# Kernel tuning notes

Measured on AMD Instinct MI355X. Metric: run time of the kernel, lower is better.

The kernel has to match this reference:

```python
import jax, jax.numpy as jnp
import numpy as np
import math

NUM_HEADS = 16
ROPE_BASE = 10000.0


def _rope_cos_sin(seq_len, head_dim, dtype):
    # Qwen2-style rotary embeddings. The torch source builds cos/sin of width
    # head_dim by concatenating freqs with itself, so the first and second
    # halves are identical; the half-width table below is the equivalent math.
    half = head_dim // 2
    inv_freq = 1.0 / (ROPE_BASE ** (jnp.arange(0, head_dim, 2, dtype=jnp.float32) / head_dim))
    t = jnp.arange(seq_len, dtype=jnp.float32)
    freqs = jnp.einsum('i,j->ij', t, inv_freq)  # [S, half]
    cos = jnp.cos(freqs).astype(dtype)[None, None]  # [1,1,S,half]
    sin = jnp.sin(freqs).astype(dtype)[None, None]
    return cos, sin


def _apply_rope(x, cos, sin):
    # x: [B, H, S, D]; split-half rotation (Qwen2 rotate-half convention)
    half = x.shape[-1] // 2
    x1, x2 = x[..., :half], x[..., half:]
    return jnp.concatenate([x1 * cos - x2 * sin, x2 * cos + x1 * sin], axis=-1)


def setup_inputs() -> dict:
    key = jax.random.key(0)
    ks = jax.random.split(key, 5)
    B, S, H = 2, 2048, 2048
    scale = 1.0 / math.sqrt(H)
    return {
        'hidden_states': jax.random.normal(ks[0], (B, S, H), dtype=jnp.float32),
        'Wq': jax.random.normal(ks[1], (H, H), dtype=jnp.float32) * scale,
        'Wk': jax.random.normal(ks[2], (H, H), dtype=jnp.float32) * scale,
        'Wv': jax.random.normal(ks[3], (H, H), dtype=jnp.float32) * scale,
        'Wo': jax.random.normal(ks[4], (H, H), dtype=jnp.float32) * scale,
    }


def reference(hidden_states, Wq, Wk, Wv, Wo):
    B, S, H = hidden_states.shape
    nh = NUM_HEADS
    hd = H // nh

    def proj(W):
        # nn.Linear: x @ W.T ; then [B,S,H] -> [B,nh,S,hd]
        y = jnp.einsum('bsh,oh->bso', hidden_states, W)
        return y.reshape(B, S, nh, hd).transpose(0, 2, 1, 3)

    q, k, v = proj(Wq), proj(Wk), proj(Wv)

    cos, sin = _rope_cos_sin(S, hd, hidden_states.dtype)
    q = _apply_rope(q, cos, sin)
    k = _apply_rope(k, cos, sin)

    scores = jnp.einsum('bhqd,bhkd->bhqk', q, k) / math.sqrt(hd)
    causal = jnp.triu(jnp.full((S, S), -jnp.inf, dtype=scores.dtype), k=1)
    scores = scores + causal[None, None]
    probs = jax.nn.softmax(scores, axis=-1)

    ctx = jnp.einsum('bhqk,bhkd->bhqd', probs, v)  # [B,nh,S,hd]
    ctx = ctx.transpose(0, 2, 1, 3).reshape(B, S, H)
    out = jnp.einsum('bsh,oh->bso', ctx, Wo)
    return out
```

## Files before the change

### kernel.cpp

```cpp
#include <hip/hip_runtime.h>

#define S_LEN 2048
#define HID   2048
#define NHEAD 16
#define HD    128
#define BSZ   2
#define BS_TOT (BSZ * S_LEN)
#define QKS   4096

typedef __bf16 bf16x8 __attribute__((ext_vector_type(8)));
typedef unsigned short u16x8 __attribute__((ext_vector_type(8)));
typedef unsigned short u16x4 __attribute__((ext_vector_type(4)));
typedef float f32x4 __attribute__((ext_vector_type(4)));

static __device__ __forceinline__ bf16x8 as_bf(u16x8 v) { return __builtin_bit_cast(bf16x8, v); }

static __device__ __forceinline__ unsigned short f2bf(float f) {
  __bf16 h = (__bf16)f;
  return __builtin_bit_cast(unsigned short, h);
}
static __device__ __forceinline__ float bf2f(unsigned short b) {
  unsigned int u = ((unsigned int)b) << 16;
  return __builtin_bit_cast(float, u);
}

static __device__ __forceinline__ void gload_lds16(const unsigned short* g, unsigned short* l) {
  __builtin_amdgcn_global_load_lds((const __attribute__((address_space(1))) unsigned int*)g,
                                   (__attribute__((address_space(3))) unsigned int*)l, 16, 0, 0);
}

__global__ __launch_bounds__(256) void cvt_all(const float* __restrict__ hs,
                                               const float* __restrict__ Wq,
                                               const float* __restrict__ Wk,
                                               const float* __restrict__ Wv,
                                               const float* __restrict__ Wo,
                                               unsigned short* __restrict__ hsb,
                                               unsigned short* __restrict__ wall,
                                               float* __restrict__ ct, float* __restrict__ st) {
  int b = (int)blockIdx.x, tid = (int)threadIdx.x;
  if (b < 8192) {
    int i = b * 256 + tid;
    float4 v = ((const float4*)hs)[i];
    ushort4 o; o.x = f2bf(v.x); o.y = f2bf(v.y); o.z = f2bf(v.z); o.w = f2bf(v.w);
    ((ushort4*)hsb)[i] = o;
  } else if (b < 24576) {
    int t = b - 8192;
    int wsel = t >> 12;
    const float* in = (wsel == 0) ? Wq : (wsel == 1) ? Wk : (wsel == 2) ? Wv : Wo;
    int i = (t & 4095) * 256 + tid;
    float4 v = ((const float4*)in)[i];
    ushort4 o; o.x = f2bf(v.x); o.y = f2bf(v.y); o.z = f2bf(v.z); o.w = f2bf(v.w);
    ((ushort4*)(wall + (size_t)wsel * HID * HID))[i] = o;
  } else {
    int id = (b - 24576) * 256 + tid;
    int tt = id >> 6, d = id & 63;
    float inv = powf(10000.0f, -(float)d * (1.0f / 64.0f));
    float f = (float)tt * inv;
    float sv, cv;
    sincosf(f, &sv, &cv);
    ct[id] = cv; st[id] = sv;
  }
}

__global__ __launch_bounds__(256) void rope_apply_k(unsigned short* __restrict__ qk,
                                                    const float* __restrict__ ct,
                                                    const float* __restrict__ st) {
  int id = blockIdx.x * 256 + threadIdx.x;
  int d4 = (id & 15) * 4;
  int h = (id >> 4) & (NHEAD - 1);
  int m = id >> 8;
  int s = m & (S_LEN - 1);
  float4 c  = *(const float4*)(ct + s * 64 + d4);
  float4 sn = *(const float4*)(st + s * 64 + d4);
  size_t base = (size_t)m * QKS + 2048 + h * HD + d4;
  u16x4 k1 = *(u16x4*)(qk + base), k2 = *(u16x4*)(qk + base + 64);
  u16x4 p1, p2;
  float cc[4] = {c.x, c.y, c.z, c.w}, ss[4] = {sn.x, sn.y, sn.z, sn.w};
#pragma unroll
  for (int j = 0; j < 4; ++j) {
    float ak = bf2f(k1[j]), bk = bf2f(k2[j]);
    p1[j] = f2bf(ak * cc[j] - bk * ss[j]);
    p2[j] = f2bf(bk * cc[j] + ak * ss[j]);
  }
  *(u16x4*)(qk + base) = p1;
  *(u16x4*)(qk + base + 64) = p2;
}

template <typename OutT>
__global__ __launch_bounds__(512, 1) void gemm256(const unsigned short* __restrict__ A,
                                                  const unsigned short* __restrict__ Bw,
                                                  OutT* __restrict__ C, int M, int N, int K) {
  __shared__ __align__(16) unsigned short As[2][256 * 64];
  __shared__ __align__(16) unsigned short Bs[2][256 * 64];
  int x = (int)blockIdx.x;
  int chunk = (int)gridDim.x >> 3;
  int x2 = (x & 7) * chunk + (x >> 3);
  const int nbn = N >> 8;
  int bm = x2 / nbn, bn = x2 % nbn;
  int tid = (int)threadIdx.x;
  int l = tid & 63, lr = l & 15, lg = l >> 4;
  int w = tid >> 6;
  int wm = w >> 2, wn = w & 3;

  int srow = 32 * w + (l >> 3);
  int sslot = (l & 7) ^ ((l >> 3) & 7);
  const unsigned short* gA = A + (size_t)(bm * 256 + srow) * K + sslot * 8;
  const unsigned short* gB = Bw + (size_t)(bn * 256 + srow) * K + sslot * 8;

  int rs7 = lr & 7;

  f32x4 zero = {0.f, 0.f, 0.f, 0.f};
  f32x4 acc[8][4];
#pragma unroll
  for (int mi = 0; mi < 8; ++mi)
#pragma unroll
    for (int ni = 0; ni < 4; ++ni) acc[mi][ni] = zero;

  int nk = K >> 6;

#define STAGE256(buf, kt)                                                       \
  do {                                                                          \
    size_t ko_ = (size_t)(kt) * 64;                                             \
    _Pragma("unroll") for (int i_ = 0; i_ < 4; ++i_) {                          \
      gload_lds16(gA + (size_t)(8 * i_) * K + ko_, &As[buf][(32 * w + 8 * i_) * 64]); \
      gload_lds16(gB + (size_t)(8 * i_) * K + ko_, &Bs[buf][(32 * w + 8 * i_) * 64]); \
    }                                                                           \
  } while (0)

  STAGE256(0, 0);
  __syncthreads();

  for (int kt = 0; kt < nk; ++kt) {
    if (kt + 1 < nk) STAGE256((kt + 1) & 1, kt + 1);
    const unsigned short* Ab = &As[kt & 1][0];
    const unsigned short* Bb = &Bs[kt & 1][0];

    u16x8 bfr[4][2];
#pragma unroll
    for (int ni = 0; ni < 4; ++ni)
#pragma unroll
      for (int ks = 0; ks < 2; ++ks)
        bfr[ni][ks] = *(const u16x8*)&Bb[(wn * 64 + ni * 16 + lr) * 64 + (((ks * 4 + lg) ^ rs7) * 8)];

#pragma unroll
    for (int mq = 0; mq < 4; ++mq) {
      u16x8 af[2][2];
#pragma unroll
      for (int m2 = 0; m2 < 2; ++m2)
#pragma unroll
        for (int ks = 0; ks < 2; ++ks)
          af[m2][ks] = *(const u16x8*)&Ab[(wm * 128 + (2 * mq + m2) * 16 + lr) * 64 + (((ks * 4 + lg) ^ rs7) * 8)];
      __builtin_amdgcn_s_setprio(1);
#pragma unroll
      for (int m2 = 0; m2 < 2; ++m2)
#pragma unroll
        for (int ni = 0; ni < 4; ++ni)
#pragma unroll
          for (int ks = 0; ks < 2; ++ks)
            acc[2 * mq + m2][ni] = __builtin_amdgcn_mfma_f32_16x16x32_bf16(
                as_bf(af[m2][ks]), as_bf(bfr[ni][ks]), acc[2 * mq + m2][ni], 0, 0, 0);
      __builtin_amdgcn_s_setprio(0);
      __builtin_amdgcn_s_barrier();
    }
    __syncthreads();
  }
#undef STAGE256

#pragma unroll
  for (int mi = 0; mi < 8; ++mi) {
#pragma unroll
    for (int ni = 0; ni < 4; ++ni) {
      int col = bn * 256 + wn * 64 + ni * 16 + lr;
#pragma unroll
      for (int j = 0; j < 4; ++j) {
        int rowm = bm * 256 + wm * 128 + mi * 16 + 4 * lg + j;
        float v = acc[mi][ni][j];
        if constexpr (sizeof(OutT) == 2) C[(size_t)rowm * N + col] = f2bf(v);
        else                             C[(size_t)rowm * N + col] = v;
      }
    }
  }
  (void)M;
}

template <typename OutT>
__global__ __launch_bounds__(256) void gemm128(const unsigned short* __restrict__ A,
                                               const unsigned short* __restrict__ Bw,
                                               OutT* __restrict__ C, int M, int N, int K) {
  __shared__ __align__(16) unsigned short As[4][128 * 32];
  __shared__ __align__(16) unsigned short Bs[4][128 * 32];
  int x = (int)blockIdx.x;
  int chunk = (int)gridDim.x >> 3;
  int x2 = (x & 7) * chunk + (x >> 3);
  const int nbn = N >> 7;
  int bm = x2 / nbn, bn = x2 % nbn;
  int tid = (int)threadIdx.x;
  int l = tid & 63, lr = l & 15, lg = l >> 4;
  int w = tid >> 6, wm = w >> 1, wn = w & 1;

  int w32 = 32 * w;
  int srow = w32 + (l >> 2);
  int ssw = ((l >> 2) ^ (l >> 4)) & 3;
  const unsigned short* gA = A + (size_t)(bm * 128 + srow) * K + (((l & 3) ^ ssw) << 3);
  const unsigned short* gB = Bw + (size_t)(bn * 128 + srow) * K + (((l & 3) ^ ssw) << 3);

  int rsw = (lr ^ (lr >> 2)) & 3;
  int aoff[4], boff[4];
#pragma unroll
  for (int i = 0; i < 4; ++i) {
    aoff[i] = (wm * 64 + i * 16 + lr) * 32 + ((lg ^ rsw) << 3);
    boff[i] = (wn * 64 + i * 16 + lr) * 32 + ((lg ^ rsw) << 3);
  }

  f32x4 zero = {0.f, 0.f, 0.f, 0.f};
  f32x4 acc[4][4];
#pragma unroll
  for (int mi = 0; mi < 4; ++mi)
#pragma unroll
    for (int ni = 0; ni < 4; ++ni) acc[mi][ni] = zero;

  int nk = K >> 5;

#define STAGE(buf, kt)                                                        \
  do {                                                                        \
    const unsigned short* pa_ = gA + (size_t)(kt) * 32;                       \
    const unsigned short* pb_ = gB + (size_t)(kt) * 32;                       \
    gload_lds16(pa_, &As[buf][w32 * 32]);                                     \
    gload_lds16(pa_ + (size_t)16 * K, &As[buf][(w32 + 16) * 32]);             \
    gload_lds16(pb_, &Bs[buf][w32 * 32]);                                     \
    gload_lds16(pb_ + (size_t)16 * K, &Bs[buf][(w32 + 16) * 32]);             \
  } while (0)

#define COMPUTE(buf)                                                          \
  do {                                                                        \
    u16x8 af[4], bfr[4];                                                      \
    _Pragma("unroll") for (int i = 0; i < 4; ++i) {                           \
      af[i] = *(const u16x8*)&As[buf][aoff[i]];                               \
      bfr[i] = *(const u16x8*)&Bs[buf][boff[i]];                              \
    }                                                                         \
    _Pragma("unroll") for (int mi = 0; mi < 4; ++mi)                          \
        _Pragma("unroll") for (int ni = 0; ni < 4; ++ni)                      \
            acc[mi][ni] = __builtin_amdgcn_mfma_f32_16x16x32_bf16(            \
                as_bf(af[mi]), as_bf(bfr[ni]), acc[mi][ni], 0, 0, 0);         \
  } while (0)

  STAGE(0, 0);
  STAGE(1, 1);
  STAGE(2, 2);
  asm volatile("s_waitcnt vmcnt(8)" ::: "memory");
  __builtin_amdgcn_s_barrier();
#pragma unroll 4
  for (int kt = 0; kt < nk; ++kt) {
    COMPUTE(kt & 3);
    asm volatile("s_waitcnt vmcnt(4) lgkmcnt(0)" ::: "memory");
    __builtin_amdgcn_s_barrier();
    STAGE((kt + 3) & 3, (kt + 3) & (nk - 1));
  }
#undef STAGE
#undef COMPUTE

#pragma unroll
  for (int mi = 0; mi < 4; ++mi) {
#pragma unroll
    for (int ni = 0; ni < 4; ++ni) {
      int col = bn * 128 + wn * 64 + ni * 16 + lr;
#pragma unroll
      for (int j = 0; j < 4; ++j) {
        int rowm = bm * 128 + wm * 64 + mi * 16 + 4 * lg + j;
        float v = acc[mi][ni][j];
        if constexpr (sizeof(OutT) == 2) C[(size_t)rowm * N + col] = f2bf(v);
        else                             C[(size_t)rowm * N + col] = v;
      }
    }
  }
  (void)M;
}

__global__ __launch_bounds__(256, 2) void attn_fwd(const unsigned short* __restrict__ qk,
                                                   const unsigned short* __restrict__ vt,
                                                   unsigned short* __restrict__ ctx,
                                                   const float* __restrict__ ct,
                                                   const float* __restrict__ st) {
  __shared__ __align__(16) unsigned short Ks[2][64 * 128];
  __shared__ __align__(16) unsigned short Vs[2][128 * 64];
  __shared__ __align__(16) unsigned short Ps[4 * 32 * 64];

  int x = (int)blockIdx.x;
  int bh, qt;
  if (x < 256) { bh = x & 31;         qt = 15 - (x >> 5); }
  else         { bh = (x - 256) & 31; qt = (x - 256) >> 5; }
  int b = bh >> 4, h = bh & 15;
  int q0 = qt * 128;
  int nt = 2 * qt + 2;

  int tid = (int)threadIdx.x;
  int w = tid >> 6, l = tid & 63, lr = l & 15, lg = l >> 4;
  const float CEXP = 0.12751744f;
  const float MB   = -23.0831391f;
  const int bS = b * S_LEN, h128 = h * HD;
  const int qw = q0 + w * 32;
  const unsigned short* qg = qk;
  const unsigned short* kg = qk + 2048;

  u16x8 qfr[2][4];
#pragma unroll
  for (int qf = 0; qf < 2; ++qf) {
    const unsigned short* qb = qg + (size_t)(bS + qw + qf * 16 + lr) * QKS + h128;
#pragma unroll
    for (int kk = 0; kk < 4; ++kk) qfr[qf][kk] = *(const u16x8*)(qb + kk * 32 + lg * 8);
    int spos = qw + qf * 16 + lr;
#pragma unroll
    for (int kk = 0; kk < 2; ++kk) {
      int d0 = kk * 32 + lg * 8;
      float4 c0 = *(const float4*)(ct + spos * 64 + d0);
      float4 c1 = *(const float4*)(ct + spos * 64 + d0 + 4);
      float4 s0 = *(const float4*)(st + spos * 64 + d0);
      float4 s1 = *(const float4*)(st + spos * 64 + d0 + 4);
      float cc[8] = {c0.x, c0.y, c0.z, c0.w, c1.x, c1.y, c1.z, c1.w};
      float sv[8] = {s0.x, s0.y, s0.z, s0.w, s1.x, s1.y, s1.z, s1.w};
      u16x8 lo = qfr[qf][kk], hi = qfr[qf][kk + 2];
#pragma unroll
      for (int j = 0; j < 8; ++j) {
        float a = bf2f(lo[j]), b2 = bf2f(hi[j]);
        lo[j] = f2bf(a * cc[j] - b2 * sv[j]);
        hi[j] = f2bf(b2 * cc[j] + a * sv[j]);
      }
      qfr[qf][kk] = lo; qfr[qf][kk + 2] = hi;
    }
  }

  const unsigned short* kbg[4];
  const unsigned short* vbg[4];
#pragma unroll
  for (int i = 0; i < 4; ++i) {
    int rr = 16 * w + 4 * i + (l >> 4);
    int colK = ((l & 15) ^ (rr & 15)) * 8;
    kbg[i] = kg + (size_t)(bS + rr) * QKS + h128 + colK;
    int vd = 32 * w + 8 * i + (l >> 3);
    int colV = ((l & 7) ^ (vd & 7)) * 8;
    vbg[i] = vt + (size_t)(h128 + vd) * BS_TOT + bS + colV;
  }

#define ASTAGE(buf, t)                                                        \
  do {                                                                        \
    size_t koff_ = (size_t)(t) * 64 * QKS;                                    \
    int voff_ = (t) * 64;                                                     \
    _Pragma("unroll") for (int i_ = 0; i_ < 4; ++i_) {                        \
      gload_lds16(kbg[i_] + koff_, &Ks[buf][(16 * w + 4 * i_) * 128]);        \
      gload_lds16(vbg[i_] + voff_, &Vs[buf][(32 * w + 8 * i_) * 64]);         \
    }                                                                         \
  } while (0)

  f32x4 zero = {0.f, 0.f, 0.f, 0.f};
  f32x4 oacc[2][8];
#pragma unroll
  for (int qf = 0; qf < 2; ++qf)
#pragma unroll
    for (int nj = 0; nj < 8; ++nj) oacc[qf][nj] = zero;
  float lsum[2] = {0.f, 0.f};

  int cur = 0;
  ASTAGE(0, 0);
  __syncthreads();

  for (int t = 0; t < nt; ++t) {
    int k0 = t * 64;
    if (t + 1 < nt) ASTAGE(cur ^ 1, t + 1);

    if (k0 <= qw + 31) {
      const unsigned short* KsB = &Ks[cur][0];
      const unsigned short* VsB = &Vs[cur][0];

      f32x4 sac[2][4];
#pragma unroll
      for (int qf = 0; qf < 2; ++qf)
#pragma unroll
        for (int ni = 0; ni < 4; ++ni) sac[qf][ni] = zero;
      __builtin_amdgcn_s_setprio(1);
#pragma unroll
      for (int kk = 0; kk < 4; ++kk) {
#pragma unroll
        for (int ni = 0; ni < 4; ++ni) {
          u16x8 kf = *(const u16x8*)&KsB[(ni * 16 + lr) * 128 + (((kk * 4 + lg) ^ lr) * 8)];
          sac[0][ni] = __builtin_amdgcn_mfma_f32_16x16x32_bf16(as_bf(kf), as_bf(qfr[0][kk]), sac[0][ni], 0, 0, 0);
          sac[1][ni] = __builtin_amdgcn_mfma_f32_16x16x32_bf16(as_bf(kf), as_bf(qfr[1][kk]), sac[1][ni], 0, 0, 0);
        }
      }
      __builtin_amdgcn_s_setprio(0);

      u16x8 vfr[2][8];
#pragma unroll
      for (int kk2 = 0; kk2 < 2; ++kk2)
#pragma unroll
        for (int nj = 0; nj < 8; ++nj)
          vfr[kk2][nj] = *(const u16x8*)&VsB[(nj * 16 + lr) * 64 + (((kk2 * 4 + lg) ^ (lr & 7)) * 8)];

      bool needmask = (k0 + 63 > qw);
      unsigned short* pw = &Ps[w * 2048];

#pragma unroll
      for (int qf = 0; qf < 2; ++qf) {
        float s[4][4];
#pragma unroll
        for (int ni = 0; ni < 4; ++ni)
#pragma unroll
          for (int j = 0; j < 4; ++j) s[ni][j] = sac[qf][ni][j];
        if (needmask) {
          int qgl = qw + qf * 16 + lr;
#pragma unroll
          for (int ni = 0; ni < 4; ++ni)
#pragma unroll
            for (int j = 0; j < 4; ++j)
              if (k0 + ni * 16 + 4 * lg + j > qgl) s[ni][j] = -1e30f;
        }
        float rs = 0.f;
#pragma unroll
        for (int ni = 0; ni < 4; ++ni)
#pragma unroll
          for (int j = 0; j < 4; ++j) {
            float p = exp2f(fmaf(s[ni][j], CEXP, MB));
            s[ni][j] = p; rs += p;
          }
        lsum[qf] += rs;
#pragma unroll
        for (int ni = 0; ni < 4; ++ni) {
          u16x4 pv = {f2bf(s[ni][0]), f2bf(s[ni][1]), f2bf(s[ni][2]), f2bf(s[ni][3])};
          *(u16x4*)&pw[(qf * 16 + lr) * 64 + (((2 * ni + (lg >> 1)) ^ (lr & 7)) * 8) + (lg & 1) * 4] = pv;
        }
        __builtin_amdgcn_s_setprio(1);
#pragma unroll
        for (int kk2 = 0; kk2 < 2; ++kk2) {
          u16x8 pa = *(const u16x8*)&pw[(qf * 16 + lr) * 64 + (((kk2 * 4 + lg) ^ (lr & 7)) * 8)];
#pragma unroll
          for (int nj = 0; nj < 8; ++nj)
            oacc[qf][nj] = __builtin_amdgcn_mfma_f32_16x16x32_bf16(as_bf(pa), as_bf(vfr[kk2][nj]), oacc[qf][nj], 0, 0, 0);
        }
        __builtin_amdgcn_s_setprio(0);
      }
    }

    __syncthreads();
    cur ^= 1;
  }
#undef ASTAGE

#pragma unroll
  for (int qf = 0; qf < 2; ++qf) {
    float ls = lsum[qf];
    ls += __shfl_xor(ls, 16);
    ls += __shfl_xor(ls, 32);
    float rl = 1.0f / ls;
    float r0 = __shfl(rl, 4 * lg + 0, 16);
    float r1 = __shfl(rl, 4 * lg + 1, 16);
    float r2 = __shfl(rl, 4 * lg + 2, 16);
    float r3 = __shfl(rl, 4 * lg + 3, 16);
    size_t obase = (size_t)(bS + qw + qf * 16 + 4 * lg) * HID + h128;
#pragma unroll
    for (int nj = 0; nj < 8; ++nj) {
      ctx[obase + 0 * HID + nj * 16 + lr] = f2bf(oacc[qf][nj][0] * r0);
      ctx[obase + 1 * HID + nj * 16 + lr] = f2bf(oacc[qf][nj][1] * r1);
      ctx[obase + 2 * HID + nj * 16 + lr] = f2bf(oacc[qf][nj][2] * r2);
      ctx[obase + 3 * HID + nj * 16 + lr] = f2bf(oacc[qf][nj][3] * r3);
    }
  }
}

extern "C" void kernel_launch(void* const* d_in, const int* in_sizes, int n_in,
                              void* d_out, int out_size, void* d_ws, size_t ws_size,
                              hipStream_t stream) {
  const float* hs = (const float*)d_in[0];
  const float* Wq = (const float*)d_in[1];
  const float* Wk = (const float*)d_in[2];
  const float* Wv = (const float*)d_in[3];
  const float* Wo = (const float*)d_in[4];

  char* ws = (char*)d_ws;
  unsigned short* hsb  = (unsigned short*)(ws);
  unsigned short* wall = (unsigned short*)(ws + 16777216);
  unsigned short* qkb  = (unsigned short*)(ws + 50331648);
  unsigned short* vtb  = (unsigned short*)(ws + 83886080);
  float* ctab = (float*)(ws + 100663296);
  float* stab = (float*)(ws + 101187584);
  unsigned short* ctxb = hsb;

  cvt_all<<<25088, 256, 0, stream>>>(hs, Wq, Wk, Wv, Wo, hsb, wall, ctab, stab);

  gemm256<unsigned short><<<256, 512, 0, stream>>>(hsb, wall, qkb, BS_TOT, 2 * HID, HID);
  gemm128<unsigned short><<<512, 256, 0, stream>>>(wall + 2 * (size_t)HID * HID, hsb, vtb, HID, BS_TOT, HID);

  rope_apply_k<<<4096, 256, 0, stream>>>(qkb, ctab, stab);

  attn_fwd<<<512, 256, 0, stream>>>(qkb, vtb, ctxb, ctab, stab);

  gemm128<float><<<512, 256, 0, stream>>>(ctxb, wall + 3 * (size_t)HID * HID, (float*)d_out, BS_TOT, HID, HID);

  (void)in_sizes; (void)n_in; (void)out_size; (void)ws_size;
}
```

Before: 270.5 us.

## Deepen GEMM pipeline to four-stage BK=32 ring with explicit vmcnt waits

Reworks the 256x256 GEMM main loop from a double-buffered BK=64 scheme into a four-buffer ring of BK=32 tiles. Three tiles are prefetched ahead, and the loop waits on vmcnt rather than a full __syncthreads, so each iteration needs only one barrier instead of several. The LDS swizzle changes to a 4-slot XOR pattern, and LDS offsets are precomputed per thread. Past the end of K the loop keeps issuing wrapped loads that are never used. It also drops the setprio hints, and the vmcnt counts must match the four loads issued per stage exactly.

```diff
diff --git a/kernel.cpp b/kernel.cpp
--- a/kernel.cpp
+++ b/kernel.cpp
@@ -90,8 +90,8 @@
 __global__ __launch_bounds__(512, 1) void gemm256(const unsigned short* __restrict__ A,
                                                   const unsigned short* __restrict__ Bw,
                                                   OutT* __restrict__ C, int M, int N, int K) {
-  __shared__ __align__(16) unsigned short As[2][256 * 64];
-  __shared__ __align__(16) unsigned short Bs[2][256 * 64];
+  __shared__ __align__(16) unsigned short As[4][256 * 32];
+  __shared__ __align__(16) unsigned short Bs[4][256 * 32];
   int x = (int)blockIdx.x;
   int chunk = (int)gridDim.x >> 3;
   int x2 = (x & 7) * chunk + (x >> 3);
@@ -102,12 +102,18 @@
   int w = tid >> 6;
   int wm = w >> 2, wn = w & 3;
 
-  int srow = 32 * w + (l >> 3);
-  int sslot = (l & 7) ^ ((l >> 3) & 7);
-  const unsigned short* gA = A + (size_t)(bm * 256 + srow) * K + sslot * 8;
-  const unsigned short* gB = Bw + (size_t)(bn * 256 + srow) * K + sslot * 8;
-
-  int rs7 = lr & 7;
+  int w32 = 32 * w;
+  int srow = w32 + (l >> 2);
+  int ssw = ((l >> 2) ^ (l >> 4)) & 3;
+  const unsigned short* gA = A + (size_t)(bm * 256 + srow) * K + (((l & 3) ^ ssw) << 3);
+  const unsigned short* gB = Bw + (size_t)(bn * 256 + srow) * K + (((l & 3) ^ ssw) << 3);
+
+  int rsw = (lr ^ (lr >> 2)) & 3;
+  int aoff[8], boff[4];
+#pragma unroll
+  for (int i = 0; i < 8; ++i) aoff[i] = (wm * 128 + i * 16 + lr) * 32 + ((lg ^ rsw) << 3);
+#pragma unroll
+  for (int i = 0; i < 4; ++i) boff[i] = (wn * 64 + i * 16 + lr) * 32 + ((lg ^ rsw) << 3);
 
   f32x4 zero = {0.f, 0.f, 0.f, 0.f};
   f32x4 acc[8][4];
@@ -116,55 +122,45 @@
 #pragma unroll
     for (int ni = 0; ni < 4; ++ni) acc[mi][ni] = zero;
 
-  int nk = K >> 6;
-
-#define STAGE256(buf, kt)                                                       \
-  do {                                                                          \
-    size_t ko_ = (size_t)(kt) * 64;                                             \
-    _Pragma("unroll") for (int i_ = 0; i_ < 4; ++i_) {                          \
-      gload_lds16(gA + (size_t)(8 * i_) * K + ko_, &As[buf][(32 * w + 8 * i_) * 64]); \
-      gload_lds16(gB + (size_t)(8 * i_) * K + ko_, &Bs[buf][(32 * w + 8 * i_) * 64]); \
-    }                                                                           \
+  int nk = K >> 5;
+
+#define STAGE(buf, kt)                                                        \
+  do {                                                                        \
+    const unsigned short* pa_ = gA + (size_t)(kt) * 32;                       \
+    const unsigned short* pb_ = gB + (size_t)(kt) * 32;                       \
+    gload_lds16(pa_, &As[buf][w32 * 32]);                                     \
+    gload_lds16(pa_ + (size_t)16 * K, &As[buf][(w32 + 16) * 32]);             \
+    gload_lds16(pb_, &Bs[buf][w32 * 32]);                                     \
+    gload_lds16(pb_ + (size_t)16 * K, &Bs[buf][(w32 + 16) * 32]);             \
   } while (0)
 
-  STAGE256(0, 0);
-  __syncthreads();
-
+#define COMPUTE(buf)                                                          \
+  do {                                                                        \
+    u16x8 bfr[4];                                                             \
+    _Pragma("unroll") for (int i = 0; i < 4; ++i)                             \
+        bfr[i] = *(const u16x8*)&Bs[buf][boff[i]];                            \
+    _Pragma("unroll") for (int mi = 0; mi < 8; ++mi) {                        \
+      u16x8 af = *(const u16x8*)&As[buf][aoff[mi]];                           \
+      _Pragma("unroll") for (int ni = 0; ni < 4; ++ni)                        \
+          acc[mi][ni] = __builtin_amdgcn_mfma_f32_16x16x32_bf16(              \
+              as_bf(af), as_bf(bfr[ni]), acc[mi][ni], 0, 0, 0);               \
+    }                                                                         \
+  } while (0)
+
+  STAGE(0, 0);
+  STAGE(1, 1);
+  STAGE(2, 2);
+  asm volatile("s_waitcnt vmcnt(8)" ::: "memory");
+  __builtin_amdgcn_s_barrier();
+#pragma unroll 4
   for (int kt = 0; kt < nk; ++kt) {
-    if (kt + 1 < nk) STAGE256((kt + 1) & 1, kt + 1);
-    const unsigned short* Ab = &As[kt & 1][0];
-    const unsigned short* Bb = &Bs[kt & 1][0];
-
-    u16x8 bfr[4][2];
-#pragma unroll
-    for (int ni = 0; ni < 4; ++ni)
-#pragma unroll
-      for (int ks = 0; ks < 2; ++ks)
-        bfr[ni][ks] = *(const u16x8*)&Bb[(wn * 64 + ni * 16 + lr) * 64 + (((ks * 4 + lg) ^ rs7) * 8)];
-
-#pragma unroll
-    for (int mq = 0; mq < 4; ++mq) {
-      u16x8 af[2][2];
-#pragma unroll
-      for (int m2 = 0; m2 < 2; ++m2)
-#pragma unroll
-        for (int ks = 0; ks < 2; ++ks)
-          af[m2][ks] = *(const u16x8*)&Ab[(wm * 128 + (2 * mq + m2) * 16 + lr) * 64 + (((ks * 4 + lg) ^ rs7) * 8)];
-      __builtin_amdgcn_s_setprio(1);
-#pragma unroll
-      for (int m2 = 0; m2 < 2; ++m2)
-#pragma unroll
-        for (int ni = 0; ni < 4; ++ni)
-#pragma unroll
-          for (int ks = 0; ks < 2; ++ks)
-            acc[2 * mq + m2][ni] = __builtin_amdgcn_mfma_f32_16x16x32_bf16(
-                as_bf(af[m2][ks]), as_bf(bfr[ni][ks]), acc[2 * mq + m2][ni], 0, 0, 0);
-      __builtin_amdgcn_s_setprio(0);
-      __builtin_amdgcn_s_barrier();
-    }
-    __syncthreads();
-  }
-#undef STAGE256
+    COMPUTE(kt & 3);
+    asm volatile("s_waitcnt vmcnt(4) lgkmcnt(0)" ::: "memory");
+    __builtin_amdgcn_s_barrier();
+    STAGE((kt + 3) & 3, (kt + 3) & (nk - 1));
+  }
+#undef STAGE
+#undef COMPUTE
 
 #pragma unroll
   for (int mi = 0; mi < 8; ++mi) {
```

Result: no change. 273.1 us (+1.0%).

## Interleave global-to-LDS loads with MFMA phases using fine-grained vmcnt waits

Applied to the files above, without the earlier changes.

Restructures the 256x256 GEMM main loop so that global-to-LDS loads for the next tiles are issued in quarter-tile chunks, one chunk per MFMA phase, instead of all at once. A partial vmcnt wait plus an s_barrier replace the full __syncthreads per k-step, and the loop is unrolled by two over the double buffer. The staging row mapping also changes so each wave loads rows from its own M half. The aim is to hide global load latency behind compute and drop a workgroup-wide barrier drain per iteration. The cost is fragile hand-counted vmcnt bookkeeping. Loads wrap around with a power-of-two mask, which produces redundant tail loads and assumes nk is a power of two.

```diff
diff --git a/kernel.cpp b/kernel.cpp
--- a/kernel.cpp
+++ b/kernel.cpp
@@ -102,12 +102,16 @@
   int w = tid >> 6;
   int wm = w >> 2, wn = w & 3;
 
-  int srow = 32 * w + (l >> 3);
-  int sslot = (l & 7) ^ ((l >> 3) & 7);
-  const unsigned short* gA = A + (size_t)(bm * 256 + srow) * K + sslot * 8;
-  const unsigned short* gB = Bw + (size_t)(bn * 256 + srow) * K + sslot * 8;
-
-  int rs7 = lr & 7;
+  int arow0 = wm * 128 + 8 * (w & 3) + (l >> 3);
+  int brow0 = 8 * w + (l >> 3);
+  int sslot = ((l & 7) ^ (l >> 3)) * 8;
+  const unsigned short* gAb = A + (size_t)(bm * 256 + arow0) * K + sslot;
+  const unsigned short* gBb = Bw + (size_t)(bn * 256 + brow0) * K + sslot;
+
+  int arw = (wm * 128 + lr) * 64;
+  int brw = (wn * 64 + lr) * 64;
+  int acol0 = ((0 + lg) ^ (lr & 7)) * 8;
+  int acol1 = ((4 + lg) ^ (lr & 7)) * 8;
 
   f32x4 zero = {0.f, 0.f, 0.f, 0.f};
   f32x4 acc[8][4];
@@ -117,54 +121,76 @@
     for (int ni = 0; ni < 4; ++ni) acc[mi][ni] = zero;
 
   int nk = K >> 6;
-
-#define STAGE256(buf, kt)                                                       \
-  do {                                                                          \
-    size_t ko_ = (size_t)(kt) * 64;                                             \
-    _Pragma("unroll") for (int i_ = 0; i_ < 4; ++i_) {                          \
-      gload_lds16(gA + (size_t)(8 * i_) * K + ko_, &As[buf][(32 * w + 8 * i_) * 64]); \
-      gload_lds16(gB + (size_t)(8 * i_) * K + ko_, &Bs[buf][(32 * w + 8 * i_) * 64]); \
-    }                                                                           \
+  int nk2 = nk >> 1;
+
+#define ISSUE_A(buf, tile, c)                                                  \
+  gload_lds16(gAb + (size_t)(32 * (c)) * K + (tile) * 64,                      \
+              &As[buf][8192 * wm + 2048 * (c) + 512 * (w & 3)])
+#define ISSUE_B(buf, tile, c)                                                  \
+  gload_lds16(gBb + (size_t)(64 * (c)) * K + (tile) * 64,                      \
+              &Bs[buf][4096 * (c) + 512 * w])
+#define HT(buf, tile, c)                                                       \
+  do { ISSUE_B(buf, tile, c); ISSUE_A(buf, tile, c); } while (0)
+#define VM6 asm volatile("s_waitcnt vmcnt(6)" ::: "memory")
+
+#define LOADB(d)                                                               \
+  do {                                                                         \
+    _Pragma("unroll") for (int ni = 0; ni < 4; ++ni) {                         \
+      bfr[ni][0] = *(const u16x8*)&Bs[d][brw + ni * 1024 + acol0];             \
+      bfr[ni][1] = *(const u16x8*)&Bs[d][brw + ni * 1024 + acol1];             \
+    }                                                                          \
   } while (0)
 
-  STAGE256(0, 0);
-  __syncthreads();
-
-  for (int kt = 0; kt < nk; ++kt) {
-    if (kt + 1 < nk) STAGE256((kt + 1) & 1, kt + 1);
-    const unsigned short* Ab = &As[kt & 1][0];
-    const unsigned short* Bb = &Bs[kt & 1][0];
-
+#define PHASE(d, q, LASTW, ...)                                                \
+  do {                                                                         \
+    u16x8 paf[2][2];                                                           \
+    _Pragma("unroll") for (int m2 = 0; m2 < 2; ++m2) {                         \
+      paf[m2][0] = *(const u16x8*)&As[d][arw + ((q) * 2 + m2) * 1024 + acol0]; \
+      paf[m2][1] = *(const u16x8*)&As[d][arw + ((q) * 2 + m2) * 1024 + acol1]; \
+    }                                                                          \
+    __VA_ARGS__;                                                               \
+    __builtin_amdgcn_sched_barrier(0);                                         \
+    __builtin_amdgcn_s_barrier();                                              \
+    __builtin_amdgcn_s_setprio(1);                                             \
+    _Pragma("unroll") for (int m2 = 0; m2 < 2; ++m2)                           \
+      _Pragma("unroll") for (int ni = 0; ni < 4; ++ni) {                       \
+        acc[(q) * 2 + m2][ni] = __builtin_amdgcn_mfma_f32_16x16x32_bf16(       \
+            as_bf(paf[m2][0]), as_bf(bfr[ni][0]), acc[(q) * 2 + m2][ni], 0, 0, 0); \
+        acc[(q) * 2 + m2][ni] = __builtin_amdgcn_mfma_f32_16x16x32_bf16(       \
+            as_bf(paf[m2][1]), as_bf(bfr[ni][1]), acc[(q) * 2 + m2][ni], 0, 0, 0); \
+      }                                                                        \
+    __builtin_amdgcn_s_setprio(0);                                             \
+    LASTW;                                                                     \
+    __builtin_amdgcn_s_barrier();                                              \
+  } while (0)
+
+  HT(0, 0, 0); HT(0, 0, 1); HT(0, 0, 2); HT(0, 0, 3);
+  HT(1, 1, 0); HT(1, 1, 1); HT(1, 1, 2);
+  VM6;
+  __builtin_amdgcn_s_barrier();
+
+  for (int t = 0; t < nk2; ++t) {
+    int Todd = 2 * t + 1;
+    int T2 = (2 * t + 2) & (nk - 1);
+    int T3 = (2 * t + 3) & (nk - 1);
     u16x8 bfr[4][2];
-#pragma unroll
-    for (int ni = 0; ni < 4; ++ni)
-#pragma unroll
-      for (int ks = 0; ks < 2; ++ks)
-        bfr[ni][ks] = *(const u16x8*)&Bb[(wn * 64 + ni * 16 + lr) * 64 + (((ks * 4 + lg) ^ rs7) * 8)];
-
-#pragma unroll
-    for (int mq = 0; mq < 4; ++mq) {
-      u16x8 af[2][2];
-#pragma unroll
-      for (int m2 = 0; m2 < 2; ++m2)
-#pragma unroll
-        for (int ks = 0; ks < 2; ++ks)
-          af[m2][ks] = *(const u16x8*)&Ab[(wm * 128 + (2 * mq + m2) * 16 + lr) * 64 + (((ks * 4 + lg) ^ rs7) * 8)];
-      __builtin_amdgcn_s_setprio(1);
-#pragma unroll
-      for (int m2 = 0; m2 < 2; ++m2)
-#pragma unroll
-        for (int ni = 0; ni < 4; ++ni)
-#pragma unroll
-          for (int ks = 0; ks < 2; ++ks)
-            acc[2 * mq + m2][ni] = __builtin_amdgcn_mfma_f32_16x16x32_bf16(
-                as_bf(af[m2][ks]), as_bf(bfr[ni][ks]), acc[2 * mq + m2][ni], 0, 0, 0);
-      __builtin_amdgcn_s_setprio(0);
-      __builtin_amdgcn_s_barrier();
-    }
-    __syncthreads();
-  }
-#undef STAGE256
+    LOADB(0);
+    PHASE(0, 0, (void)0, HT(1, Todd, 3));
+    PHASE(0, 1, (void)0, HT(0, T2, 0));
+    PHASE(0, 2, (void)0, HT(0, T2, 1));
+    PHASE(0, 3, VM6,     HT(0, T2, 2));
+    LOADB(1);
+    PHASE(1, 0, (void)0, HT(0, T2, 3));
+    PHASE(1, 1, (void)0, HT(1, T3, 0));
+    PHASE(1, 2, (void)0, HT(1, T3, 1));
+    PHASE(1, 3, VM6,     HT(1, T3, 2));
+  }
+#undef PHASE
+#undef LOADB
+#undef VM6
+#undef HT
+#undef ISSUE_A
+#undef ISSUE_B
 
 #pragma unroll
   for (int mi = 0; mi < 8; ++mi) {
```

Result: faster. 263.6 us (median of 3 runs) (-2.6%).
